# Optimization experiments

Measured on AMD Instinct MI355X. Metric: run time of the kernel, lower is better.

## Reference

```python
import jax, jax.numpy as jnp
import numpy as np

N_NODES = 50000
N_EDGES = 800000
DIM = 128
LN_EPS = 1e-5


def setup_inputs() -> dict:
    key = jax.random.key(0)
    k1, k2, k3, k4, k5 = jax.random.split(key, 5)
    x = jax.random.normal(k1, (N_NODES, DIM), dtype=jnp.float32)
    edge_index = jax.random.randint(k2, (2, N_EDGES), 0, N_NODES, dtype=jnp.int64)
    edge_weight = jax.random.uniform(k3, (N_EDGES,), dtype=jnp.float32)
    # GCNConv linear (PyG Linear: out = x @ W.T + b)
    W = jax.random.normal(k4, (DIM, DIM), dtype=jnp.float32) / np.sqrt(DIM)
    b = jnp.zeros((DIM,), dtype=jnp.float32)
    # pygnn.LayerNorm(dim, mode='node') affine params
    ln_weight = jnp.ones((DIM,), dtype=jnp.float32)
    ln_bias = jnp.zeros((DIM,), dtype=jnp.float32)
    return {"x": x, "edge_index": edge_index, "edge_weight": edge_weight,
            "W": W, "b": b, "ln_weight": ln_weight, "ln_bias": ln_bias}


def reference(x, edge_index, edge_weight, W, b, ln_weight, ln_bias):
    n = x.shape[0]
    # --- LayerNorm (mode='node'): per-node over feature dim ---
    mu = jnp.mean(x, axis=-1, keepdims=True)
    var = jnp.mean(jnp.square(x - mu), axis=-1, keepdims=True)
    xn = (x - mu) * jax.lax.rsqrt(var + LN_EPS) * ln_weight + ln_bias
    # --- GCNConv: linear first, then normalized propagate ---
    h = xn @ W.T  # [N, dim]
    row, col = edge_index[0], edge_index[1]  # source, target
    # add self loops (fill_value = 1.0)
    loop = jnp.arange(n, dtype=edge_index.dtype)
    row_f = jnp.concatenate([row, loop])
    col_f = jnp.concatenate([col, loop])
    ew_f = jnp.concatenate([edge_weight, jnp.ones((n,), dtype=edge_weight.dtype)])
    # symmetric gcn normalization: deg over target (col)
    deg = jax.ops.segment_sum(ew_f, col_f, num_segments=n)
    dinv = jnp.where(deg > 0, jax.lax.rsqrt(deg), 0.0)
    norm = dinv[row_f] * ew_f * dinv[col_f]  # [E+N]
    # gather-scale-scatter
    msg = h[row_f] * norm[:, None]  # [E+N, dim]
    out = jax.ops.segment_sum(msg, col_f, num_segments=n) + b
    # --- GELU (torch default = exact erf form); dropout is identity (p=0 / eval) ---
    return jax.nn.gelu(out, approximate=False)
```

## Files before the change

### kernel.cpp

```cpp
#include <hip/hip_runtime.h>
#include <math.h>

#define DIM 128
#define LN_EPS 1e-5f
#define HB 512
#define CAP 2048

typedef __attribute__((ext_vector_type(8))) short short8;
typedef __attribute__((ext_vector_type(4))) float floatx4;

__device__ __forceinline__ float gelu_exact(float v) {
    return 0.5f * v * (1.0f + erff(v * 0.70710678118654752f));
}
__device__ __forceinline__ float bf2f(unsigned short u) {
    return __uint_as_float(((unsigned)u) << 16);
}
__device__ __forceinline__ short f2bf(float f) {
    unsigned b = __float_as_uint(f);
    return (short)((b + 0x7FFF + ((b >> 16) & 1)) >> 16);
}

__global__ __launch_bounds__(256) void gemm_hist_kernel(
    const float* __restrict__ x, const float* __restrict__ W,
    const float* __restrict__ lnw, const float* __restrict__ lnb,
    unsigned short* __restrict__ h16,
    const int* __restrict__ col, int* __restrict__ hist,
    int n, int E, int nbkt)
{
    __shared__ short swb[2048 * 8];
    __shared__ short axb[1024 * 8];
    const int tid = threadIdx.x;

    if ((int)blockIdx.x < HB) {
        int* lh = (int*)swb;
        for (int b = tid; b < nbkt; b += 256) lh[b] = 0;
        __syncthreads();
        int g = blockIdx.x;
        int chunk = (E + HB - 1) / HB;
        int e0 = g * chunk;
        int e1 = e0 + chunk; if (e1 > E) e1 = E;
        for (int e = e0 + tid; e < e1; e += 256)
            atomicAdd(&lh[col[e] >> 6], 1);
        __syncthreads();
        for (int b = tid; b < nbkt; b += 256)
            hist[(size_t)g * nbkt + b] = lh[b];
        return;
    }

    const int gb = blockIdx.x - HB;
    const int n0 = gb * 64;

    for (int c = tid; c < 2048; c += 256) {
        int nrow = ((c >> 8) << 4) | (c & 15);
        int kb   = (((c >> 6) & 3) << 5) + (((c >> 4) & 3) << 3);
        const float* wp = W + nrow * DIM + kb;
        float4 w0 = *(const float4*)wp;
        float4 w1 = *(const float4*)(wp + 4);
        short8 p;
        p[0] = f2bf(w0.x); p[1] = f2bf(w0.y); p[2] = f2bf(w0.z); p[3] = f2bf(w0.w);
        p[4] = f2bf(w1.x); p[5] = f2bf(w1.y); p[6] = f2bf(w1.z); p[7] = f2bf(w1.w);
        *(short8*)&swb[c * 8] = p;
    }

    {
        int m = tid >> 2, sub = tid & 3;
        int node = n0 + m;
        bool valid = (node < n);
        const float4* xp = (const float4*)(x + (size_t)node * DIM + sub * 32);
        float4 v[8];
        float s = 0.f, ss = 0.f;
        #pragma unroll
        for (int i = 0; i < 8; ++i) {
            v[i] = valid ? xp[i] : make_float4(0.f, 0.f, 0.f, 0.f);
            s  += v[i].x + v[i].y + v[i].z + v[i].w;
            ss += v[i].x * v[i].x + v[i].y * v[i].y + v[i].z * v[i].z + v[i].w * v[i].w;
        }
        s += __shfl_xor(s, 1); ss += __shfl_xor(ss, 1);
        s += __shfl_xor(s, 2); ss += __shfl_xor(ss, 2);
        float mu   = s * (1.0f / 128.0f);
        float var  = ss * (1.0f / 128.0f) - mu * mu;
        float rstd = rsqrtf(var + LN_EPS);

        int mt = m >> 4, mloc = m & 15;
        #pragma unroll
        for (int quad = 0; quad < 4; ++quad) {
            float4 a = v[2 * quad], c4 = v[2 * quad + 1];
            const float4* lw = (const float4*)(lnw + sub * 32 + quad * 8);
            const float4* lb = (const float4*)(lnb + sub * 32 + quad * 8);
            float4 lw0 = lw[0], lw1 = lw[1], lb0 = lb[0], lb1 = lb[1];
            short8 p;
            p[0] = f2bf((a.x  - mu) * rstd * lw0.x + lb0.x);
            p[1] = f2bf((a.y  - mu) * rstd * lw0.y + lb0.y);
            p[2] = f2bf((a.z  - mu) * rstd * lw0.z + lb0.z);
            p[3] = f2bf((a.w  - mu) * rstd * lw0.w + lb0.w);
            p[4] = f2bf((c4.x - mu) * rstd * lw1.x + lb1.x);
            p[5] = f2bf((c4.y - mu) * rstd * lw1.y + lb1.y);
            p[6] = f2bf((c4.z - mu) * rstd * lw1.z + lb1.z);
            p[7] = f2bf((c4.w - mu) * rstd * lw1.w + lb1.w);
            int slot = mt * 256 + sub * 64 + quad * 16 + mloc;
            *(short8*)&axb[slot * 8] = p;
        }
    }
    __syncthreads();

    const int w    = tid >> 6;
    const int lane = tid & 63;

    short8 afrag[4];
    #pragma unroll
    for (int kq = 0; kq < 4; ++kq)
        afrag[kq] = *(const short8*)&axb[(w * 256 + kq * 64 + lane) * 8];

    floatx4 acc[8];
    #pragma unroll
    for (int jt = 0; jt < 8; ++jt) acc[jt] = (floatx4){0.f, 0.f, 0.f, 0.f};

    #pragma unroll
    for (int jt = 0; jt < 8; ++jt) {
        #pragma unroll
        for (int kq = 0; kq < 4; ++kq) {
            short8 bfrag = *(const short8*)&swb[(jt * 256 + kq * 64 + lane) * 8];
            acc[jt] = __builtin_amdgcn_mfma_f32_16x16x32_bf16(afrag[kq], bfrag,
                                                              acc[jt], 0, 0, 0);
        }
    }

    const int quad = lane >> 4, nl = lane & 15;
    #pragma unroll
    for (int jt = 0; jt < 8; ++jt) {
        #pragma unroll
        for (int r = 0; r < 4; ++r) {
            int rnode = n0 + w * 16 + quad * 4 + r;
            if (rnode < n)
                h16[(size_t)rnode * DIM + jt * 16 + nl] = (unsigned short)f2bf(acc[jt][r]);
        }
    }
}

__global__ __launch_bounds__(256) void expand_kernel(
    const int* __restrict__ hist, int* __restrict__ base,
    int* __restrict__ cnt, int nbkt)
{
    __shared__ int ls[256];
    const int tid = threadIdx.x;
    const int b = blockIdx.x;

    int v0 = hist[(size_t)(2 * tid)     * nbkt + b];
    int v1 = hist[(size_t)(2 * tid + 1) * nbkt + b];
    int p = v0 + v1;
    ls[tid] = p;
    __syncthreads();
    int inc = p;
    for (int off = 1; off < 256; off <<= 1) {
        int add = (tid >= off) ? ls[tid - off] : 0;
        __syncthreads();
        inc += add;
        ls[tid] = inc;
        __syncthreads();
    }
    int ex = inc - p;
    int a0 = b * CAP + ex;
    base[(size_t)(2 * tid)     * nbkt + b] = a0;
    base[(size_t)(2 * tid + 1) * nbkt + b] = a0 + v0;
    if (tid == 255) cnt[b] = inc;
}

__global__ __launch_bounds__(256) void bucket_scatter_kernel(
    const int* __restrict__ row, const int* __restrict__ col,
    const float* __restrict__ ew, const int* __restrict__ base,
    int2* __restrict__ srt, int E, int nbkt)
{
    __shared__ int cur[1024];
    const int tid = threadIdx.x, g = blockIdx.x;
    for (int b = tid; b < nbkt; b += 256)
        cur[b] = base[(size_t)g * nbkt + b];
    __syncthreads();
    int chunk = (E + HB - 1) / HB;
    int e0 = g * chunk;
    int e1 = e0 + chunk; if (e1 > E) e1 = E;
    for (int e = e0 + tid; e < e1; e += 256) {
        int c = col[e];
        int pos = atomicAdd(&cur[c >> 6], 1);
        srt[pos] = make_int2(((c & 63) << 16) | row[e], __float_as_int(ew[e]));
    }
}

__global__ __launch_bounds__(256) void dinv_kernel(
    const int2* __restrict__ srt, const int* __restrict__ cnt,
    float* __restrict__ dinv, int n)
{
    __shared__ float w64[64];
    const int tid = threadIdx.x, b = blockIdx.x;
    if (tid < 64) w64[tid] = 0.f;
    __syncthreads();
    int c = cnt[b];
    int s0 = b * CAP;
    for (int i = tid; i < c; i += 256) {
        int2 v = srt[s0 + i];
        atomicAdd(&w64[(v.x >> 16) & 63], __int_as_float(v.y));
    }
    __syncthreads();
    if (tid < 64)
        dinv[b * 64 + tid] = rsqrtf(1.0f + w64[tid]);
}

__global__ __launch_bounds__(256) void bucket_gather_kernel(
    const int2* __restrict__ srt, const int* __restrict__ cnt,
    const float* __restrict__ dinv, const unsigned short* __restrict__ h16,
    const float* __restrict__ bias, float* __restrict__ out, int n)
{
    __shared__ int2  bufA[CAP];
    __shared__ int2  bufB[CAP];
    __shared__ int   k64[64], off64[64], cur64[64];
    __shared__ float di64[64];
    const int tid = threadIdx.x, b = blockIdx.x;

    if (tid < 64) { k64[tid] = 0; di64[tid] = dinv[b * 64 + tid]; }
    __syncthreads();

    const int c  = cnt[b];
    const int s0 = b * CAP;
    const int grp = tid >> 4;
    const int sub = tid & 15;

    if (c <= CAP) {
        for (int i = tid; i < c; i += 256) {
            int2 v = srt[s0 + i];
            bufA[i] = v;
            atomicAdd(&k64[(v.x >> 16) & 63], 1);
        }
        __syncthreads();
        if (tid == 0) {
            int run = 0;
            #pragma unroll
            for (int d = 0; d < 64; ++d) { off64[d] = run; cur64[d] = run; run += k64[d]; }
        }
        __syncthreads();
        for (int i = tid; i < c; i += 256) {
            int2 v = bufA[i];
            int d   = (v.x >> 16) & 63;
            int src = v.x & 0xFFFF;
            float nrm = dinv[src] * __int_as_float(v.y) * di64[d];
            int p = atomicAdd(&cur64[d], 1);
            bufB[p] = make_int2(src, __float_as_int(nrm));
        }
        __syncthreads();

        #pragma unroll
        for (int dd = 0; dd < 4; ++dd) {
            int d = dd * 16 + grp;
            int dest = b * 64 + d;
            if (dest >= n) continue;
            float di = di64[d];
            short8 sv = *(const short8*)(h16 + (size_t)dest * DIM + sub * 8);
            float s2 = di * di;
            float acc[8];
            #pragma unroll
            for (int k = 0; k < 8; ++k) acc[k] = s2 * bf2f((unsigned short)sv[k]);

            int j  = off64[d];
            int je = j + k64[d];
            for (; j + 3 < je; j += 4) {
                int2 e0 = bufB[j],     e1 = bufB[j + 1];
                int2 e2 = bufB[j + 2], e3 = bufB[j + 3];
                short8 a0 = *(const short8*)(h16 + (size_t)e0.x * DIM + sub * 8);
                short8 a1 = *(const short8*)(h16 + (size_t)e1.x * DIM + sub * 8);
                short8 a2 = *(const short8*)(h16 + (size_t)e2.x * DIM + sub * 8);
                short8 a3 = *(const short8*)(h16 + (size_t)e3.x * DIM + sub * 8);
                float n0 = __int_as_float(e0.y);
                float n1 = __int_as_float(e1.y);
                float n2 = __int_as_float(e2.y);
                float n3 = __int_as_float(e3.y);
                #pragma unroll
                for (int k = 0; k < 8; ++k) {
                    acc[k] = fmaf(n0, bf2f((unsigned short)a0[k]), acc[k]);
                    acc[k] = fmaf(n1, bf2f((unsigned short)a1[k]), acc[k]);
                    acc[k] = fmaf(n2, bf2f((unsigned short)a2[k]), acc[k]);
                    acc[k] = fmaf(n3, bf2f((unsigned short)a3[k]), acc[k]);
                }
            }
            for (; j < je; ++j) {
                int2 e0 = bufB[j];
                float n0 = __int_as_float(e0.y);
                short8 a = *(const short8*)(h16 + (size_t)e0.x * DIM + sub * 8);
                #pragma unroll
                for (int k = 0; k < 8; ++k)
                    acc[k] = fmaf(n0, bf2f((unsigned short)a[k]), acc[k]);
            }

            float4 b0 = *(const float4*)(bias + sub * 8);
            float4 b1 = *(const float4*)(bias + sub * 8 + 4);
            float4 o0, o1;
            o0.x = gelu_exact(acc[0] + b0.x); o0.y = gelu_exact(acc[1] + b0.y);
            o0.z = gelu_exact(acc[2] + b0.z); o0.w = gelu_exact(acc[3] + b0.w);
            o1.x = gelu_exact(acc[4] + b1.x); o1.y = gelu_exact(acc[5] + b1.y);
            o1.z = gelu_exact(acc[6] + b1.z); o1.w = gelu_exact(acc[7] + b1.w);
            float* op = out + (size_t)dest * DIM + sub * 8;
            *(float4*)op       = o0;
            *(float4*)(op + 4) = o1;
        }
    } else {
        #pragma unroll
        for (int dd = 0; dd < 4; ++dd) {
            int d = dd * 16 + grp;
            int dest = b * 64 + d;
            if (dest >= n) continue;
            float di = di64[d];
            short8 sv = *(const short8*)(h16 + (size_t)dest * DIM + sub * 8);
            float s2 = di * di;
            float acc[8];
            #pragma unroll
            for (int k = 0; k < 8; ++k) acc[k] = s2 * bf2f((unsigned short)sv[k]);
            for (int i = 0; i < c; ++i) {
                int2 v = srt[s0 + i];
                if (((v.x >> 16) & 63) != d) continue;
                int src = v.x & 0xFFFF;
                float nrm = dinv[src] * __int_as_float(v.y) * di;
                short8 a = *(const short8*)(h16 + (size_t)src * DIM + sub * 8);
                #pragma unroll
                for (int k = 0; k < 8; ++k)
                    acc[k] = fmaf(nrm, bf2f((unsigned short)a[k]), acc[k]);
            }
            float4 b0 = *(const float4*)(bias + sub * 8);
            float4 b1 = *(const float4*)(bias + sub * 8 + 4);
            float4 o0, o1;
            o0.x = gelu_exact(acc[0] + b0.x); o0.y = gelu_exact(acc[1] + b0.y);
            o0.z = gelu_exact(acc[2] + b0.z); o0.w = gelu_exact(acc[3] + b0.w);
            o1.x = gelu_exact(acc[4] + b1.x); o1.y = gelu_exact(acc[5] + b1.y);
            o1.z = gelu_exact(acc[6] + b1.z); o1.w = gelu_exact(acc[7] + b1.w);
            float* op = out + (size_t)dest * DIM + sub * 8;
            *(float4*)op       = o0;
            *(float4*)(op + 4) = o1;
        }
    }
}

extern "C" void kernel_launch(void* const* d_in, const int* in_sizes, int n_in,
                              void* d_out, int out_size, void* d_ws, size_t ws_size,
                              hipStream_t stream)
{
    const float* x    = (const float*)d_in[0];
    const int*   ei   = (const int*)d_in[1];
    const float* ew   = (const float*)d_in[2];
    const float* W    = (const float*)d_in[3];
    const float* b    = (const float*)d_in[4];
    const float* ln_w = (const float*)d_in[5];
    const float* ln_b = (const float*)d_in[6];
    float* out = (float*)d_out;

    const int n = in_sizes[0] / DIM;
    const int E = in_sizes[2];
    const int* row  = ei;
    const int* colp = ei + E;
    const int nbkt = (n + 63) / 64;

    int2*           srt  = (int2*)d_ws;
    unsigned short* h16  = (unsigned short*)(srt + (size_t)nbkt * CAP);
    int*            hist = (int*)(h16 + (size_t)n * DIM);
    int*            base = hist + (size_t)HB * nbkt;
    int*            cnt  = base + (size_t)HB * nbkt;
    float*          dinv = (float*)(cnt + nbkt);

    const int GB = (n + 63) / 64;

    gemm_hist_kernel<<<HB + GB, 256, 0, stream>>>(x, W, ln_w, ln_b, h16,
                                                  colp, hist, n, E, nbkt);
    expand_kernel<<<nbkt, 256, 0, stream>>>(hist, base, cnt, nbkt);
    bucket_scatter_kernel<<<HB, 256, 0, stream>>>(row, colp, ew, base, srt, E, nbkt);
    dinv_kernel<<<nbkt, 256, 0, stream>>>(srt, cnt, dinv, n);
    bucket_gather_kernel<<<nbkt, 256, 0, stream>>>(srt, cnt, dinv, h16, b, out, n);
}
```

Before: 171.0 us.

## Fuse pipeline phases into one cooperative persistent kernel with grid syncs

Replaces the five separate launches with one cooperative persistent kernel that runs histogram+GEMM, expand, scatter, dinv and gather as phases separated by grid.sync, keeping a multi-launch fallback. It also pre-converts W into bf16 MFMA fragments once in a small separate kernel and reads them from global memory instead of rebuilding them in LDS in every GEMM block. GEMM outputs are staged through LDS so that h16 is written with coalesced 16-byte stores. This is meant to cut launch gaps and redundant W conversion, at the cost of grid-sync overhead, a fixed grid capped at 1024 blocks, and B-fragment reads from global/L2 instead of LDS.

```diff
diff --git a/kernel.cpp b/kernel.cpp
--- a/kernel.cpp
+++ b/kernel.cpp
@@ -1,10 +1,14 @@
 #include <hip/hip_runtime.h>
+#include <hip/hip_cooperative_groups.h>
 #include <math.h>
+
+namespace cg = cooperative_groups;
 
 #define DIM 128
 #define LN_EPS 1e-5f
 #define HB 512
 #define CAP 2048
+#define SMEM_BYTES 34816
 
 typedef __attribute__((ext_vector_type(8))) short short8;
 typedef __attribute__((ext_vector_type(4))) float floatx4;
@@ -20,47 +24,49 @@
     return (short)((b + 0x7FFF + ((b >> 16) & 1)) >> 16);
 }
 
-__global__ __launch_bounds__(256) void gemm_hist_kernel(
-    const float* __restrict__ x, const float* __restrict__ W,
+__global__ __launch_bounds__(256) void wconv_kernel(
+    const float* __restrict__ W, short* __restrict__ wfrag)
+{
+    int c = blockIdx.x * 256 + threadIdx.x;
+    int nrow = ((c >> 8) << 4) | (c & 15);
+    int kb   = (((c >> 6) & 3) << 5) + (((c >> 4) & 3) << 3);
+    const float* wp = W + nrow * DIM + kb;
+    float4 w0 = *(const float4*)wp;
+    float4 w1 = *(const float4*)(wp + 4);
+    short8 p;
+    p[0] = f2bf(w0.x); p[1] = f2bf(w0.y); p[2] = f2bf(w0.z); p[3] = f2bf(w0.w);
+    p[4] = f2bf(w1.x); p[5] = f2bf(w1.y); p[6] = f2bf(w1.z); p[7] = f2bf(w1.w);
+    *(short8*)&wfrag[c * 8] = p;
+}
+
+
+__device__ __forceinline__ void ph_hist(
+    char* smem, int g, const int* __restrict__ col, int* __restrict__ hist,
+    int E, int nbkt, int tid)
+{
+    int* lh = (int*)smem;
+    __syncthreads();
+    for (int b = tid; b < nbkt; b += 256) lh[b] = 0;
+    __syncthreads();
+    int chunk = (E + HB - 1) / HB;
+    int e0 = g * chunk;
+    int e1 = e0 + chunk; if (e1 > E) e1 = E;
+    for (int e = e0 + tid; e < e1; e += 256)
+        atomicAdd(&lh[col[e] >> 6], 1);
+    __syncthreads();
+    for (int b = tid; b < nbkt; b += 256)
+        hist[(size_t)g * nbkt + b] = lh[b];
+}
+
+__device__ __forceinline__ void ph_gemm(
+    char* smem, int gb, const float* __restrict__ x,
+    const short8* __restrict__ wf,
     const float* __restrict__ lnw, const float* __restrict__ lnb,
-    unsigned short* __restrict__ h16,
-    const int* __restrict__ col, int* __restrict__ hist,
-    int n, int E, int nbkt)
-{
-    __shared__ short swb[2048 * 8];
-    __shared__ short axb[1024 * 8];
-    const int tid = threadIdx.x;
-
-    if ((int)blockIdx.x < HB) {
-        int* lh = (int*)swb;
-        for (int b = tid; b < nbkt; b += 256) lh[b] = 0;
-        __syncthreads();
-        int g = blockIdx.x;
-        int chunk = (E + HB - 1) / HB;
-        int e0 = g * chunk;
-        int e1 = e0 + chunk; if (e1 > E) e1 = E;
-        for (int e = e0 + tid; e < e1; e += 256)
-            atomicAdd(&lh[col[e] >> 6], 1);
-        __syncthreads();
-        for (int b = tid; b < nbkt; b += 256)
-            hist[(size_t)g * nbkt + b] = lh[b];
-        return;
-    }
-
-    const int gb = blockIdx.x - HB;
+    unsigned short* __restrict__ h16, int n, int tid)
+{
+    short* axb = (short*)smem;
+    __syncthreads();
     const int n0 = gb * 64;
-
-    for (int c = tid; c < 2048; c += 256) {
-        int nrow = ((c >> 8) << 4) | (c & 15);
-        int kb   = (((c >> 6) & 3) << 5) + (((c >> 4) & 3) << 3);
-        const float* wp = W + nrow * DIM + kb;
-        float4 w0 = *(const float4*)wp;
-        float4 w1 = *(const float4*)(wp + 4);
-        short8 p;
-        p[0] = f2bf(w0.x); p[1] = f2bf(w0.y); p[2] = f2bf(w0.z); p[3] = f2bf(w0.w);
-        p[4] = f2bf(w1.x); p[5] = f2bf(w1.y); p[6] = f2bf(w1.z); p[7] = f2bf(w1.w);
-        *(short8*)&swb[c * 8] = p;
-    }
 
     {
         int m = tid >> 2, sub = tid & 3;
@@ -119,32 +125,41 @@
     for (int jt = 0; jt < 8; ++jt) {
         #pragma unroll
         for (int kq = 0; kq < 4; ++kq) {
-            short8 bfrag = *(const short8*)&swb[(jt * 256 + kq * 64 + lane) * 8];
+            short8 bfrag = wf[jt * 256 + kq * 64 + lane];
             acc[jt] = __builtin_amdgcn_mfma_f32_16x16x32_bf16(afrag[kq], bfrag,
                                                               acc[jt], 0, 0, 0);
         }
     }
+    __syncthreads();
 
     const int quad = lane >> 4, nl = lane & 15;
+    const int HS = 136;
+    short* hb = (short*)smem;
     #pragma unroll
     for (int jt = 0; jt < 8; ++jt) {
         #pragma unroll
-        for (int r = 0; r < 4; ++r) {
-            int rnode = n0 + w * 16 + quad * 4 + r;
-            if (rnode < n)
-                h16[(size_t)rnode * DIM + jt * 16 + nl] = (unsigned short)f2bf(acc[jt][r]);
-        }
-    }
-}
-
-__global__ __launch_bounds__(256) void expand_kernel(
-    const int* __restrict__ hist, int* __restrict__ base,
-    int* __restrict__ cnt, int nbkt)
-{
-    __shared__ int ls[256];
-    const int tid = threadIdx.x;
-    const int b = blockIdx.x;
-
+        for (int r = 0; r < 4; ++r)
+            hb[(w * 16 + quad * 4 + r) * HS + jt * 16 + nl] = f2bf(acc[jt][r]);
+    }
+    __syncthreads();
+    {
+        int rrow = tid >> 2, seg = tid & 3;
+        int node = n0 + rrow;
+        if (node < n) {
+            const short8* sp = (const short8*)&hb[rrow * HS + seg * 32];
+            short8 v0 = sp[0], v1 = sp[1], v2 = sp[2], v3 = sp[3];
+            short8* dp = (short8*)(h16 + (size_t)node * DIM + seg * 32);
+            dp[0] = v0; dp[1] = v1; dp[2] = v2; dp[3] = v3;
+        }
+    }
+}
+
+__device__ __forceinline__ void ph_expand(
+    char* smem, int b, const int* __restrict__ hist, int* __restrict__ base,
+    int* __restrict__ cnt, int nbkt, int tid)
+{
+    int* ls = (int*)smem;
+    __syncthreads();
     int v0 = hist[(size_t)(2 * tid)     * nbkt + b];
     int v1 = hist[(size_t)(2 * tid + 1) * nbkt + b];
     int p = v0 + v1;
@@ -165,13 +180,13 @@
     if (tid == 255) cnt[b] = inc;
 }
 
-__global__ __launch_bounds__(256) void bucket_scatter_kernel(
-    const int* __restrict__ row, const int* __restrict__ col,
+__device__ __forceinline__ void ph_scatter(
+    char* smem, int g, const int* __restrict__ row, const int* __restrict__ col,
     const float* __restrict__ ew, const int* __restrict__ base,
-    int2* __restrict__ srt, int E, int nbkt)
-{
-    __shared__ int cur[1024];
-    const int tid = threadIdx.x, g = blockIdx.x;
+    int2* __restrict__ srt, int E, int nbkt, int tid)
+{
+    int* cur = (int*)smem;
+    __syncthreads();
     for (int b = tid; b < nbkt; b += 256)
         cur[b] = base[(size_t)g * nbkt + b];
     __syncthreads();
@@ -185,12 +200,12 @@
     }
 }
 
-__global__ __launch_bounds__(256) void dinv_kernel(
-    const int2* __restrict__ srt, const int* __restrict__ cnt,
-    float* __restrict__ dinv, int n)
-{
-    __shared__ float w64[64];
-    const int tid = threadIdx.x, b = blockIdx.x;
+__device__ __forceinline__ void ph_dinv(
+    char* smem, int b, const int2* __restrict__ srt, const int* __restrict__ cnt,
+    float* __restrict__ dinv, int tid)
+{
+    float* w64 = (float*)smem;
+    __syncthreads();
     if (tid < 64) w64[tid] = 0.f;
     __syncthreads();
     int c = cnt[b];
@@ -204,16 +219,18 @@
         dinv[b * 64 + tid] = rsqrtf(1.0f + w64[tid]);
 }
 
-__global__ __launch_bounds__(256) void bucket_gather_kernel(
-    const int2* __restrict__ srt, const int* __restrict__ cnt,
+__device__ __forceinline__ void ph_gather(
+    char* smem, int b, const int2* __restrict__ srt, const int* __restrict__ cnt,
     const float* __restrict__ dinv, const unsigned short* __restrict__ h16,
-    const float* __restrict__ bias, float* __restrict__ out, int n)
-{
-    __shared__ int2  bufA[CAP];
-    __shared__ int2  bufB[CAP];
-    __shared__ int   k64[64], off64[64], cur64[64];
-    __shared__ float di64[64];
-    const int tid = threadIdx.x, b = blockIdx.x;
+    const float* __restrict__ bias, float* __restrict__ out, int n, int tid)
+{
+    int2*  bufA  = (int2*)smem;
+    int2*  bufB  = (int2*)(smem + 16384);
+    int*   k64   = (int*)(smem + 32768);
+    int*   off64 = (int*)(smem + 32768 + 256);
+    int*   cur64 = (int*)(smem + 32768 + 512);
+    float* di64  = (float*)(smem + 32768 + 768);
+    __syncthreads();
 
     if (tid < 64) { k64[tid] = 0; di64[tid] = dinv[b * 64 + tid]; }
     __syncthreads();
@@ -335,6 +352,85 @@
     }
 }
 
+__global__ __launch_bounds__(256) void mega_kernel(
+    const float* __restrict__ x, const short* __restrict__ wfrag,
+    const float* __restrict__ lnw, const float* __restrict__ lnb,
+    unsigned short* __restrict__ h16,
+    const int* __restrict__ row, const int* __restrict__ col,
+    const float* __restrict__ ew,
+    int* __restrict__ hist, int* __restrict__ base, int* __restrict__ cnt,
+    int2* __restrict__ srt, float* __restrict__ dinv,
+    float* __restrict__ out, const float* __restrict__ bias,
+    int n, int E, int nbkt)
+{
+    __shared__ __align__(16) char smem[SMEM_BYTES];
+    cg::grid_group grid = cg::this_grid();
+    const int tid = threadIdx.x;
+    const int GBt = (n + 63) / 64;
+
+    for (int t = blockIdx.x; t < HB + GBt; t += gridDim.x) {
+        if (t < HB) ph_hist(smem, t, col, hist, E, nbkt, tid);
+        else        ph_gemm(smem, t - HB, x, (const short8*)wfrag, lnw, lnb,
+                            h16, n, tid);
+    }
+    grid.sync();
+    for (int t = blockIdx.x; t < nbkt; t += gridDim.x)
+        ph_expand(smem, t, hist, base, cnt, nbkt, tid);
+    grid.sync();
+    for (int t = blockIdx.x; t < HB; t += gridDim.x)
+        ph_scatter(smem, t, row, col, ew, base, srt, E, nbkt, tid);
+    grid.sync();
+    for (int t = blockIdx.x; t < nbkt; t += gridDim.x)
+        ph_dinv(smem, t, srt, cnt, dinv, tid);
+    grid.sync();
+    for (int t = blockIdx.x; t < nbkt; t += gridDim.x)
+        ph_gather(smem, t, srt, cnt, dinv, h16, bias, out, n, tid);
+}
+
+__global__ __launch_bounds__(256) void k_phaseA(
+    const float* __restrict__ x, const short* __restrict__ wfrag,
+    const float* __restrict__ lnw, const float* __restrict__ lnb,
+    unsigned short* __restrict__ h16, const int* __restrict__ col,
+    int* __restrict__ hist, int n, int E, int nbkt)
+{
+    __shared__ __align__(16) char smem[SMEM_BYTES];
+    if ((int)blockIdx.x < HB)
+        ph_hist(smem, blockIdx.x, col, hist, E, nbkt, threadIdx.x);
+    else
+        ph_gemm(smem, blockIdx.x - HB, x, (const short8*)wfrag, lnw, lnb,
+                h16, n, threadIdx.x);
+}
+__global__ __launch_bounds__(256) void k_expand(
+    const int* __restrict__ hist, int* __restrict__ base,
+    int* __restrict__ cnt, int nbkt)
+{
+    __shared__ __align__(16) char smem[SMEM_BYTES];
+    ph_expand(smem, blockIdx.x, hist, base, cnt, nbkt, threadIdx.x);
+}
+__global__ __launch_bounds__(256) void k_scatter(
+    const int* __restrict__ row, const int* __restrict__ col,
+    const float* __restrict__ ew, const int* __restrict__ base,
+    int2* __restrict__ srt, int E, int nbkt)
+{
+    __shared__ __align__(16) char smem[SMEM_BYTES];
+    ph_scatter(smem, blockIdx.x, row, col, ew, base, srt, E, nbkt, threadIdx.x);
+}
+__global__ __launch_bounds__(256) void k_dinv(
+    const int2* __restrict__ srt, const int* __restrict__ cnt,
+    float* __restrict__ dinv)
+{
+    __shared__ __align__(16) char smem[SMEM_BYTES];
+    ph_dinv(smem, blockIdx.x, srt, cnt, dinv, threadIdx.x);
+}
+__global__ __launch_bounds__(256) void k_gather(
+    const int2* __restrict__ srt, const int* __restrict__ cnt,
+    const float* __restrict__ dinv, const unsigned short* __restrict__ h16,
+    const float* __restrict__ bias, float* __restrict__ out, int n)
+{
+    __shared__ __align__(16) char smem[SMEM_BYTES];
+    ph_gather(smem, blockIdx.x, srt, cnt, dinv, h16, bias, out, n, threadIdx.x);
+}
+
 extern "C" void kernel_launch(void* const* d_in, const int* in_sizes, int n_in,
                               void* d_out, int out_size, void* d_ws, size_t ws_size,
                               hipStream_t stream)
@@ -354,19 +450,58 @@
     const int* colp = ei + E;
     const int nbkt = (n + 63) / 64;
 
-    int2*           srt  = (int2*)d_ws;
-    unsigned short* h16  = (unsigned short*)(srt + (size_t)nbkt * CAP);
-    int*            hist = (int*)(h16 + (size_t)n * DIM);
-    int*            base = hist + (size_t)HB * nbkt;
-    int*            cnt  = base + (size_t)HB * nbkt;
-    float*          dinv = (float*)(cnt + nbkt);
+    int2*           srt   = (int2*)d_ws;
+    unsigned short* h16   = (unsigned short*)(srt + (size_t)nbkt * CAP);
+    short*          wfrag = (short*)(h16 + (size_t)n * DIM);
+    int*            hist  = (int*)(wfrag + 16384);
+    int*            base  = hist + (size_t)HB * nbkt;
+    int*            cnt   = base + (size_t)HB * nbkt;
+    float*          dinv  = (float*)(cnt + nbkt);
 
     const int GB = (n + 63) / 64;
 
-    gemm_hist_kernel<<<HB + GB, 256, 0, stream>>>(x, W, ln_w, ln_b, h16,
-                                                  colp, hist, n, E, nbkt);
-    expand_kernel<<<nbkt, 256, 0, stream>>>(hist, base, cnt, nbkt);
-    bucket_scatter_kernel<<<HB, 256, 0, stream>>>(row, colp, ew, base, srt, E, nbkt);
-    dinv_kernel<<<nbkt, 256, 0, stream>>>(srt, cnt, dinv, n);
-    bucket_gather_kernel<<<nbkt, 256, 0, stream>>>(srt, cnt, dinv, h16, b, out, n);
-}
+    wconv_kernel<<<8, 256, 0, stream>>>(W, wfrag);
+
+    static int s_grid = 0;
+    if (s_grid == 0) {
+        int dev = 0;
+        (void)hipGetDevice(&dev);
+        int ncu = 256;
+        (void)hipDeviceGetAttribute(&ncu, hipDeviceAttributeMultiprocessorCount, dev);
+        int bpc = 0;
+        (void)hipOccupancyMaxActiveBlocksPerMultiprocessor(
+            &bpc, (const void*)mega_kernel, 256, 0);
+        if (bpc < 1) bpc = 1;
+        long g = (long)ncu * bpc;
+        if (g > 1024) g = 1024;
+        if (g < 1) g = 1;
+        s_grid = (int)g;
+    }
+
+    static bool s_coop_ok = true;
+    bool launched = false;
+    if (s_coop_ok) {
+        void* args[] = {
+            (void*)&x, (void*)&wfrag, (void*)&ln_w, (void*)&ln_b, (void*)&h16,
+            (void*)&row, (void*)&colp, (void*)&ew,
+            (void*)&hist, (void*)&base, (void*)&cnt,
+            (void*)&srt, (void*)&dinv, (void*)&out, (void*)&b,
+            (void*)&n, (void*)&E, (void*)&nbkt };
+        hipError_t err = hipLaunchCooperativeKernel(
+            (const void*)mega_kernel, dim3(s_grid), dim3(256), args, 0, stream);
+        if (err == hipSuccess) {
+            launched = true;
+        } else {
+            (void)hipGetLastError();
+            s_coop_ok = false;
+        }
+    }
+    if (!launched) {
+        k_phaseA<<<HB + GB, 256, 0, stream>>>(x, wfrag, ln_w, ln_b, h16,
+                                              colp, hist, n, E, nbkt);
+        k_expand<<<nbkt, 256, 0, stream>>>(hist, base, cnt, nbkt);
+        k_scatter<<<HB, 256, 0, stream>>>(row, colp, ew, base, srt, E, nbkt);
+        k_dinv<<<nbkt, 256, 0, stream>>>(srt, cnt, dinv);
+        k_gather<<<nbkt, 256, 0, stream>>>(srt, cnt, dinv, h16, b, out, n);
+    }
+}
```

New measurement: 388.9 us. +127.5%, slower.

## Precompute bf16 W fragments once and stage GEMM output through LDS

Applied to the files above, without the earlier changes.

Moves the per-block fp32-to-bf16 conversion and swizzle of W into a small separate kernel that writes MFMA-ready fragments to workspace. The GEMM blocks then read B fragments straight from global memory/cache instead of rebuilding them in LDS. Shared memory shrinks to one reused buffer, which may raise occupancy. The output tile is staged in padded LDS so h16 is written with wide coalesced row stores instead of scattered 2-byte stores. The cost is an extra kernel launch and global-memory fragment loads inside the MFMA loop.

```diff
diff --git a/kernel.cpp b/kernel.cpp
--- a/kernel.cpp
+++ b/kernel.cpp
@@ -20,19 +20,33 @@
     return (short)((b + 0x7FFF + ((b >> 16) & 1)) >> 16);
 }
 
+__global__ __launch_bounds__(256) void wconv_kernel(
+    const float* __restrict__ W, short* __restrict__ wfrag)
+{
+    int c = blockIdx.x * 256 + threadIdx.x;
+    int nrow = ((c >> 8) << 4) | (c & 15);
+    int kb   = (((c >> 6) & 3) << 5) + (((c >> 4) & 3) << 3);
+    const float* wp = W + nrow * DIM + kb;
+    float4 w0 = *(const float4*)wp;
+    float4 w1 = *(const float4*)(wp + 4);
+    short8 p;
+    p[0] = f2bf(w0.x); p[1] = f2bf(w0.y); p[2] = f2bf(w0.z); p[3] = f2bf(w0.w);
+    p[4] = f2bf(w1.x); p[5] = f2bf(w1.y); p[6] = f2bf(w1.z); p[7] = f2bf(w1.w);
+    *(short8*)&wfrag[c * 8] = p;
+}
+
 __global__ __launch_bounds__(256) void gemm_hist_kernel(
-    const float* __restrict__ x, const float* __restrict__ W,
+    const float* __restrict__ x, const short* __restrict__ wfrag,
     const float* __restrict__ lnw, const float* __restrict__ lnb,
     unsigned short* __restrict__ h16,
     const int* __restrict__ col, int* __restrict__ hist,
     int n, int E, int nbkt)
 {
-    __shared__ short swb[2048 * 8];
-    __shared__ short axb[1024 * 8];
+    __shared__ short ubuf[8448];
     const int tid = threadIdx.x;
 
     if ((int)blockIdx.x < HB) {
-        int* lh = (int*)swb;
+        int* lh = (int*)ubuf;
         for (int b = tid; b < nbkt; b += 256) lh[b] = 0;
         __syncthreads();
         int g = blockIdx.x;
@@ -49,18 +63,7 @@
 
     const int gb = blockIdx.x - HB;
     const int n0 = gb * 64;
-
-    for (int c = tid; c < 2048; c += 256) {
-        int nrow = ((c >> 8) << 4) | (c & 15);
-        int kb   = (((c >> 6) & 3) << 5) + (((c >> 4) & 3) << 3);
-        const float* wp = W + nrow * DIM + kb;
-        float4 w0 = *(const float4*)wp;
-        float4 w1 = *(const float4*)(wp + 4);
-        short8 p;
-        p[0] = f2bf(w0.x); p[1] = f2bf(w0.y); p[2] = f2bf(w0.z); p[3] = f2bf(w0.w);
-        p[4] = f2bf(w1.x); p[5] = f2bf(w1.y); p[6] = f2bf(w1.z); p[7] = f2bf(w1.w);
-        *(short8*)&swb[c * 8] = p;
-    }
+    short* axb = ubuf;
 
     {
         int m = tid >> 2, sub = tid & 3;
@@ -105,11 +108,13 @@
 
     const int w    = tid >> 6;
     const int lane = tid & 63;
+    const short8* wf = (const short8*)wfrag;
 
     short8 afrag[4];
     #pragma unroll
     for (int kq = 0; kq < 4; ++kq)
         afrag[kq] = *(const short8*)&axb[(w * 256 + kq * 64 + lane) * 8];
+    __syncthreads();
 
     floatx4 acc[8];
     #pragma unroll
@@ -119,20 +124,30 @@
     for (int jt = 0; jt < 8; ++jt) {
         #pragma unroll
         for (int kq = 0; kq < 4; ++kq) {
-            short8 bfrag = *(const short8*)&swb[(jt * 256 + kq * 64 + lane) * 8];
+            short8 bfrag = wf[jt * 256 + kq * 64 + lane];
             acc[jt] = __builtin_amdgcn_mfma_f32_16x16x32_bf16(afrag[kq], bfrag,
                                                               acc[jt], 0, 0, 0);
         }
     }
 
     const int quad = lane >> 4, nl = lane & 15;
+    const int HS = 132;
+    short* hb = ubuf;
     #pragma unroll
     for (int jt = 0; jt < 8; ++jt) {
         #pragma unroll
-        for (int r = 0; r < 4; ++r) {
-            int rnode = n0 + w * 16 + quad * 4 + r;
-            if (rnode < n)
-                h16[(size_t)rnode * DIM + jt * 16 + nl] = (unsigned short)f2bf(acc[jt][r]);
+        for (int r = 0; r < 4; ++r)
+            hb[(w * 16 + quad * 4 + r) * HS + jt * 16 + nl] = f2bf(acc[jt][r]);
+    }
+    __syncthreads();
+    {
+        int rrow = tid >> 2, seg = tid & 3;
+        int node = n0 + rrow;
+        if (node < n) {
+            const short8* sp = (const short8*)&hb[rrow * HS + seg * 32];
+            short8 v0 = sp[0], v1 = sp[1], v2 = sp[2], v3 = sp[3];
+            short8* dp = (short8*)(h16 + (size_t)node * DIM + seg * 32);
+            dp[0] = v0; dp[1] = v1; dp[2] = v2; dp[3] = v3;
         }
     }
 }
@@ -354,16 +369,18 @@
     const int* colp = ei + E;
     const int nbkt = (n + 63) / 64;
 
-    int2*           srt  = (int2*)d_ws;
-    unsigned short* h16  = (unsigned short*)(srt + (size_t)nbkt * CAP);
-    int*            hist = (int*)(h16 + (size_t)n * DIM);
-    int*            base = hist + (size_t)HB * nbkt;
-    int*            cnt  = base + (size_t)HB * nbkt;
-    float*          dinv = (float*)(cnt + nbkt);
+    int2*           srt   = (int2*)d_ws;
+    unsigned short* h16   = (unsigned short*)(srt + (size_t)nbkt * CAP);
+    short*          wfrag = (short*)(h16 + (size_t)n * DIM);
+    int*            hist  = (int*)(wfrag + 16384);
+    int*            base  = hist + (size_t)HB * nbkt;
+    int*            cnt   = base + (size_t)HB * nbkt;
+    float*          dinv  = (float*)(cnt + nbkt);
 
     const int GB = (n + 63) / 64;
 
-    gemm_hist_kernel<<<HB + GB, 256, 0, stream>>>(x, W, ln_w, ln_b, h16,
+    wconv_kernel<<<8, 256, 0, stream>>>(W, wfrag);
+    gemm_hist_kernel<<<HB + GB, 256, 0, stream>>>(x, wfrag, ln_w, ln_b, h16,
                                                   colp, hist, n, E, nbkt);
     expand_kernel<<<nbkt, 256, 0, stream>>>(hist, base, cnt, nbkt);
     bucket_scatter_kernel<<<HB, 256, 0, stream>>>(row, colp, ew, base, srt, E, nbkt);
```

New measurement: 173.7 us. About the same (+1.6%).

## Prescale h by source dinv, stage GEMM output via LDS, parallelize bucket scan

Applied to the files above, without the earlier changes.

Folds the source-side dinv factor into h16 during the dinv pass, so the gather no longer does a random dinv[src] lookup per edge and applies the destination dinv once at the end. The GEMM epilogue now stages bf16 results in LDS and writes rows with coalesced 16-byte stores instead of scattered 2-byte stores. It also replaces the serial single-thread prefix sum over 64 destinations with a wavefront shuffle scan. The cost is an extra read-modify-write pass over h16 and a second bf16 rounding of h, which adds error.

```diff
diff --git a/kernel.cpp b/kernel.cpp
--- a/kernel.cpp
+++ b/kernel.cpp
@@ -28,11 +28,11 @@
     int n, int E, int nbkt)
 {
     __shared__ short swb[2048 * 8];
-    __shared__ short axb[1024 * 8];
+    __shared__ short ubuf[8448];
     const int tid = threadIdx.x;
 
     if ((int)blockIdx.x < HB) {
-        int* lh = (int*)swb;
+        int* lh = (int*)ubuf;
         for (int b = tid; b < nbkt; b += 256) lh[b] = 0;
         __syncthreads();
         int g = blockIdx.x;
@@ -49,6 +49,7 @@
 
     const int gb = blockIdx.x - HB;
     const int n0 = gb * 64;
+    short* axb = ubuf;
 
     for (int c = tid; c < 2048; c += 256) {
         int nrow = ((c >> 8) << 4) | (c & 15);
@@ -110,6 +111,7 @@
     #pragma unroll
     for (int kq = 0; kq < 4; ++kq)
         afrag[kq] = *(const short8*)&axb[(w * 256 + kq * 64 + lane) * 8];
+    __syncthreads();
 
     floatx4 acc[8];
     #pragma unroll
@@ -126,13 +128,23 @@
     }
 
     const int quad = lane >> 4, nl = lane & 15;
+    const int HS = 132;
+    short* hb = ubuf;
     #pragma unroll
     for (int jt = 0; jt < 8; ++jt) {
         #pragma unroll
-        for (int r = 0; r < 4; ++r) {
-            int rnode = n0 + w * 16 + quad * 4 + r;
-            if (rnode < n)
-                h16[(size_t)rnode * DIM + jt * 16 + nl] = (unsigned short)f2bf(acc[jt][r]);
+        for (int r = 0; r < 4; ++r)
+            hb[(w * 16 + quad * 4 + r) * HS + jt * 16 + nl] = f2bf(acc[jt][r]);
+    }
+    __syncthreads();
+    {
+        int rrow = tid >> 2, seg = tid & 3;
+        int node = n0 + rrow;
+        if (node < n) {
+            const short8* sp = (const short8*)&hb[rrow * HS + seg * 32];
+            short8 v0 = sp[0], v1 = sp[1], v2 = sp[2], v3 = sp[3];
+            short8* dp = (short8*)(h16 + (size_t)node * DIM + seg * 32);
+            dp[0] = v0; dp[1] = v1; dp[2] = v2; dp[3] = v3;
         }
     }
 }
@@ -185,11 +197,12 @@
     }
 }
 
-__global__ __launch_bounds__(256) void dinv_kernel(
+__global__ __launch_bounds__(256) void dinv_scale_kernel(
     const int2* __restrict__ srt, const int* __restrict__ cnt,
-    float* __restrict__ dinv, int n)
+    float* __restrict__ dinv, unsigned short* __restrict__ h16, int n)
 {
     __shared__ float w64[64];
+    __shared__ float di64s[64];
     const int tid = threadIdx.x, b = blockIdx.x;
     if (tid < 64) w64[tid] = 0.f;
     __syncthreads();
@@ -200,8 +213,27 @@
         atomicAdd(&w64[(v.x >> 16) & 63], __int_as_float(v.y));
     }
     __syncthreads();
-    if (tid < 64)
-        dinv[b * 64 + tid] = rsqrtf(1.0f + w64[tid]);
+    if (tid < 64) {
+        float dv = rsqrtf(1.0f + w64[tid]);
+        di64s[tid] = dv;
+        dinv[b * 64 + tid] = dv;
+    }
+    __syncthreads();
+    int rrow = tid >> 2, seg = tid & 3;
+    int node = b * 64 + rrow;
+    if (node < n) {
+        float dv = di64s[rrow];
+        short8* p = (short8*)(h16 + (size_t)node * DIM + seg * 32);
+        #pragma unroll
+        for (int q = 0; q < 4; ++q) {
+            short8 v = p[q];
+            short8 o;
+            #pragma unroll
+            for (int k = 0; k < 8; ++k)
+                o[k] = f2bf(dv * bf2f((unsigned short)v[k]));
+            p[q] = o;
+        }
+    }
 }
 
 __global__ __launch_bounds__(256) void bucket_gather_kernel(
@@ -230,19 +262,23 @@
             atomicAdd(&k64[(v.x >> 16) & 63], 1);
         }
         __syncthreads();
-        if (tid == 0) {
-            int run = 0;
+        if (tid < 64) {
+            int v = k64[tid];
+            int inc = v;
             #pragma unroll
-            for (int d = 0; d < 64; ++d) { off64[d] = run; cur64[d] = run; run += k64[d]; }
+            for (int off = 1; off < 64; off <<= 1) {
+                int t = __shfl_up(inc, off, 64);
+                if (tid >= off) inc += t;
+            }
+            off64[tid] = inc - v;
+            cur64[tid] = inc - v;
         }
         __syncthreads();
         for (int i = tid; i < c; i += 256) {
             int2 v = bufA[i];
-            int d   = (v.x >> 16) & 63;
-            int src = v.x & 0xFFFF;
-            float nrm = dinv[src] * __int_as_float(v.y) * di64[d];
+            int d = (v.x >> 16) & 63;
             int p = atomicAdd(&cur64[d], 1);
-            bufB[p] = make_int2(src, __float_as_int(nrm));
+            bufB[p] = make_int2(v.x & 0xFFFF, v.y);
         }
         __syncthreads();
 
@@ -253,10 +289,9 @@
             if (dest >= n) continue;
             float di = di64[d];
             short8 sv = *(const short8*)(h16 + (size_t)dest * DIM + sub * 8);
-            float s2 = di * di;
             float acc[8];
             #pragma unroll
-            for (int k = 0; k < 8; ++k) acc[k] = s2 * bf2f((unsigned short)sv[k]);
+            for (int k = 0; k < 8; ++k) acc[k] = bf2f((unsigned short)sv[k]);
 
             int j  = off64[d];
             int je = j + k64[d];
@@ -291,10 +326,10 @@
             float4 b0 = *(const float4*)(bias + sub * 8);
             float4 b1 = *(const float4*)(bias + sub * 8 + 4);
             float4 o0, o1;
-            o0.x = gelu_exact(acc[0] + b0.x); o0.y = gelu_exact(acc[1] + b0.y);
-            o0.z = gelu_exact(acc[2] + b0.z); o0.w = gelu_exact(acc[3] + b0.w);
-            o1.x = gelu_exact(acc[4] + b1.x); o1.y = gelu_exact(acc[5] + b1.y);
-            o1.z = gelu_exact(acc[6] + b1.z); o1.w = gelu_exact(acc[7] + b1.w);
+            o0.x = gelu_exact(di * acc[0] + b0.x); o0.y = gelu_exact(di * acc[1] + b0.y);
+            o0.z = gelu_exact(di * acc[2] + b0.z); o0.w = gelu_exact(di * acc[3] + b0.w);
+            o1.x = gelu_exact(di * acc[4] + b1.x); o1.y = gelu_exact(di * acc[5] + b1.y);
+            o1.z = gelu_exact(di * acc[6] + b1.z); o1.w = gelu_exact(di * acc[7] + b1.w);
             float* op = out + (size_t)dest * DIM + sub * 8;
             *(float4*)op       = o0;
             *(float4*)(op + 4) = o1;
@@ -307,27 +342,26 @@
             if (dest >= n) continue;
             float di = di64[d];
             short8 sv = *(const short8*)(h16 + (size_t)dest * DIM + sub * 8);
-            float s2 = di * di;
             float acc[8];
             #pragma unroll
-            for (int k = 0; k < 8; ++k) acc[k] = s2 * bf2f((unsigned short)sv[k]);
+            for (int k = 0; k < 8; ++k) acc[k] = bf2f((unsigned short)sv[k]);
             for (int i = 0; i < c; ++i) {
                 int2 v = srt[s0 + i];
                 if (((v.x >> 16) & 63) != d) continue;
                 int src = v.x & 0xFFFF;
-                float nrm = dinv[src] * __int_as_float(v.y) * di;
+                float n0 = __int_as_float(v.y);
                 short8 a = *(const short8*)(h16 + (size_t)src * DIM + sub * 8);
                 #pragma unroll
                 for (int k = 0; k < 8; ++k)
-                    acc[k] = fmaf(nrm, bf2f((unsigned short)a[k]), acc[k]);
+                    acc[k] = fmaf(n0, bf2f((unsigned short)a[k]), acc[k]);
             }
             float4 b0 = *(const float4*)(bias + sub * 8);
             float4 b1 = *(const float4*)(bias + sub * 8 + 4);
             float4 o0, o1;
-            o0.x = gelu_exact(acc[0] + b0.x); o0.y = gelu_exact(acc[1] + b0.y);
-            o0.z = gelu_exact(acc[2] + b0.z); o0.w = gelu_exact(acc[3] + b0.w);
-            o1.x = gelu_exact(acc[4] + b1.x); o1.y = gelu_exact(acc[5] + b1.y);
-            o1.z = gelu_exact(acc[6] + b1.z); o1.w = gelu_exact(acc[7] + b1.w);
+            o0.x = gelu_exact(di * acc[0] + b0.x); o0.y = gelu_exact(di * acc[1] + b0.y);
+            o0.z = gelu_exact(di * acc[2] + b0.z); o0.w = gelu_exact(di * acc[3] + b0.w);
+            o1.x = gelu_exact(di * acc[4] + b1.x); o1.y = gelu_exact(di * acc[5] + b1.y);
+            o1.z = gelu_exact(di * acc[6] + b1.z); o1.w = gelu_exact(di * acc[7] + b1.w);
             float* op = out + (size_t)dest * DIM + sub * 8;
             *(float4*)op       = o0;
             *(float4*)(op + 4) = o1;
@@ -367,6 +401,6 @@
                                                   colp, hist, n, E, nbkt);
     expand_kernel<<<nbkt, 256, 0, stream>>>(hist, base, cnt, nbkt);
     bucket_scatter_kernel<<<HB, 256, 0, stream>>>(row, colp, ew, base, srt, E, nbkt);
-    dinv_kernel<<<nbkt, 256, 0, stream>>>(srt, cnt, dinv, n);
+    dinv_scale_kernel<<<nbkt, 256, 0, stream>>>(srt, cnt, dinv, h16, n);
     bucket_gather_kernel<<<nbkt, 256, 0, stream>>>(srt, cnt, dinv, h16, b, out, n);
 }
```

Result: slower. 179.4 us (+5.0%).
